# Kernel optimization log

Measured on AMD Instinct MI355X. Metric: run time of the kernel, lower is better.

## Reference

```python
import jax, jax.numpy as jnp
import numpy as np

B, N, T, F_IN, K, NUM_CLASSES = 32, 62, 1024, 5, 9, 3
CH = [F_IN, 32, 64, 128]
STRIDES = [1, 2, 1]
EPS = 1e-5  # torch InstanceNorm2d default eps


def setup_inputs() -> dict:
    key = jax.random.key(0)
    ks = jax.random.split(key, 32)
    ctr = [0]
    def nxt():
        k = ks[ctr[0]]; ctr[0] += 1; return k
    def nrm(shape, fan_in):
        return jax.random.normal(nxt(), shape, dtype=jnp.float32) / np.float32(np.sqrt(fan_in))
    inp = {}
    inp["x"] = jax.random.normal(nxt(), (B, N, T, F_IN), dtype=jnp.float32)
    # frozen learned graph: symmetric, non-negative, sparse-ish, zero diagonal
    a = jax.random.uniform(nxt(), (N, N), dtype=jnp.float32)
    a = jnp.maximum(jnp.tanh(a + a.T), 0.0)
    a = jnp.where(a > 0.8, a, 0.0)
    inp["adj"] = a * (1.0 - jnp.eye(N, dtype=jnp.float32))
    for i in range(3):
        cin, cout = CH[i], CH[i + 1]
        inp[f"gcn_w{i}"] = nrm((cin, cout), cin)
        inp[f"gcn_b{i}"] = jnp.zeros((cout,), jnp.float32)
        inp[f"conv_w{i}"] = nrm((cout, cout, 1, K), cout * K)
        inp[f"conv_b{i}"] = jnp.zeros((cout,), jnp.float32)
        inp[f"res_w{i}"] = nrm((cout, cin, 1, 1), cin)
        inp[f"res_b{i}"] = jnp.zeros((cout,), jnp.float32)
    inp["attn_w1"] = nrm((128, 64), 128)
    inp["attn_b1"] = jnp.zeros((64,), jnp.float32)
    inp["attn_w2"] = nrm((64, 1), 64)
    inp["attn_b2"] = jnp.zeros((1,), jnp.float32)
    inp["fc_w"] = nrm((128, NUM_CLASSES), 128)
    inp["fc_b"] = jnp.zeros((NUM_CLASSES,), jnp.float32)
    return inp


def _instance_norm(x):
    # InstanceNorm2d, affine=False: normalize per (sample, channel) over (node, time)
    m = jnp.mean(x, axis=(2, 3), keepdims=True)
    v = jnp.mean(jnp.square(x - m), axis=(2, 3), keepdims=True)
    return (x - m) * jax.lax.rsqrt(v + EPS)


def _conv(x, w, b, stride, pad):
    y = jax.lax.conv_general_dilated(
        x, w, window_strides=(1, stride), padding=[(0, 0), (pad, pad)],
        dimension_numbers=("NCHW", "OIHW", "NCHW"))
    return y + b[None, :, None, None]


def _block(x, a_norm, wg, bg, wc, bc, wr, br, stride):
    # residual 1x1 conv (always present: in!=out for every block here)
    res = _conv(x, wr, br, stride, 0)
    # GCNConv over all (batch, time) slices at once: A_norm @ (X W) + b
    y = jnp.einsum("bfnt,fo->bont", x, wg)
    y = jnp.einsum("mn,bont->bomt", a_norm, y) + bg[None, :, None, None]
    # TCN: IN -> ReLU -> Conv(1,K) -> IN -> ReLU (dropout = identity in eval)
    y = jax.nn.relu(_instance_norm(y))
    y = _conv(y, wc, bc, stride, (K - 1) // 2)
    y = jax.nn.relu(_instance_norm(y))
    return jax.nn.relu(y + res)


def _forward(x, adj, params, attn_w1, attn_b1, attn_w2, attn_b2, fc_w, fc_b):
    # symmetric GCN normalization with self loops (PyG gcn_norm on dense support)
    a_hat = adj + jnp.eye(N, dtype=adj.dtype)
    d = jnp.sum(a_hat, axis=1)
    dinv = jnp.where(d > 0, jax.lax.rsqrt(jnp.maximum(d, EPS)), 0.0)
    a_norm = dinv[:, None] * a_hat * dinv[None, :]
    h = jnp.transpose(x, (0, 3, 1, 2))  # (B, F, N, T)
    for i in range(3):
        h = _block(h, a_norm, *params[i], STRIDES[i])
    h = jnp.transpose(jnp.mean(h, axis=2), (0, 2, 1))  # (B, T', 128)
    hid = jnp.tanh(h @ attn_w1 + attn_b1)
    score = (hid @ attn_w2)[..., 0] + attn_b2[0]      # (B, T')
    w = jax.nn.softmax(score, axis=1)
    feat = jnp.einsum("btf,bt->bf", h, w)
    logits = feat @ fc_w + fc_b
    return logits, adj


def reference(x, adj,
              gcn_w0, gcn_b0, conv_w0, conv_b0, res_w0, res_b0,
              gcn_w1, gcn_b1, conv_w1, conv_b1, res_w1, res_b1,
              gcn_w2, gcn_b2, conv_w2, conv_b2, res_w2, res_b2,
              attn_w1, attn_b1, attn_w2, attn_b2, fc_w, fc_b):
    params = [
        (gcn_w0, gcn_b0, conv_w0, conv_b0, res_w0, res_b0),
        (gcn_w1, gcn_b1, conv_w1, conv_b1, res_w1, res_b1),
        (gcn_w2, gcn_b2, conv_w2, conv_b2, res_w2, res_b2),
    ]
    return _forward(x, adj, params, attn_w1, attn_b1, attn_w2, attn_b2, fc_w, fc_b)
```

## Files before the change

### kernel.cpp

```cpp
#include <hip/hip_runtime.h>


#define NN 62
#define KK 9

typedef short s16x8 __attribute__((ext_vector_type(8)));
typedef float f32x4 __attribute__((ext_vector_type(4)));

__device__ __forceinline__ unsigned short f2bf(float f) {
  unsigned u = __builtin_bit_cast(unsigned, f);
  u += 0x7FFF + ((u >> 16) & 1);
  return (unsigned short)(u >> 16);
}
__device__ __forceinline__ float bf2f(unsigned short u) {
  unsigned v = ((unsigned)u) << 16;
  return __builtin_bit_cast(float, v);
}
__device__ __forceinline__ ushort4 pack4(float4 a) {
  return (ushort4){f2bf(a.x), f2bf(a.y), f2bf(a.z), f2bf(a.w)};
}

__global__ __launch_bounds__(256) void k_prep(const float* __restrict__ adj,
                                              float* __restrict__ a_norm,
                                              float* __restrict__ out_adj) {
  __shared__ float dinv[NN];
  int tid = threadIdx.x;
  if (tid < NN) {
    float s = 1.0f;
    for (int n = 0; n < NN; n++) s += adj[tid * NN + n];
    dinv[tid] = (s > 0.f) ? rsqrtf(fmaxf(s, 1e-5f)) : 0.f;
  }
  __syncthreads();
  for (int idx = tid; idx < NN * NN; idx += 256) {
    int m = idx / NN, n = idx - m * NN;
    float ah = adj[idx] + ((m == n) ? 1.f : 0.f);
    a_norm[idx] = dinv[m] * ah * dinv[n];
    out_adj[idx] = adj[idx];
  }
}

__global__ __launch_bounds__(256) void k_an(const float* __restrict__ a_norm,
                                            unsigned short* __restrict__ anf) {
  int idx = blockIdx.x * 256 + threadIdx.x;
  if (idx >= 4096) return;
  int j = idx & 7;
  int l = (idx >> 3) & 63;
  int rest = idx >> 9;
  int cb = rest & 1;
  int ob = rest >> 1;
  int m = ob * 16 + (l & 15);
  int n = cb * 32 + (l >> 4) * 8 + j;
  anf[idx] = (m < NN && n < NN) ? f2bf(a_norm[m * NN + n]) : (unsigned short)0;
}

__global__ __launch_bounds__(256) void k_wt(const float* __restrict__ wc,
                                            unsigned short* __restrict__ wf, int C,
                                            const float* __restrict__ wr,
                                            float* __restrict__ wrt, int CIN) {
  int stride = gridDim.x * blockDim.x;
  int total = KK * C * C;
  int nCB = C / 32;
  for (int idx = blockIdx.x * blockDim.x + threadIdx.x; idx < total; idx += stride) {
    int j = idx & 7;
    int l = (idx >> 3) & 63;
    int rest = idx >> 9;
    int cb = rest % nCB;
    int rest2 = rest / nCB;
    int ob = rest2 % (C / 16);
    int k = rest2 / (C / 16);
    int o = ob * 16 + (l & 15);
    int ci = cb * 32 + (l >> 4) * 8 + j;
    wf[idx] = f2bf(wc[((size_t)o * C + ci) * KK + k]);
  }
  int t2 = C * CIN;
  for (int i = blockIdx.x * blockDim.x + threadIdx.x; i < t2; i += stride) {
    int o = i / CIN, ci = i - o * CIN;
    wrt[ci * C + o] = wr[i];
  }
}

__global__ __launch_bounds__(256) void k_wg(const float* __restrict__ gw,
                                            unsigned short* __restrict__ wgf,
                                            int CIN, int COUT, int KPAD) {
  int total = (COUT / 16) * (KPAD / 32) * 512;
  int stride = gridDim.x * blockDim.x;
  for (int idx = blockIdx.x * blockDim.x + threadIdx.x; idx < total; idx += stride) {
    int j = idx & 7;
    int l = (idx >> 3) & 63;
    int rest = idx >> 9;
    int cb = rest % (KPAD / 32);
    int ob = rest / (KPAD / 32);
    int o = ob * 16 + (l & 15);
    int f = cb * 32 + (l >> 4) * 8 + j;
    wgf[idx] = (f < CIN) ? f2bf(gw[(size_t)f * COUT + o]) : (unsigned short)0;
  }
}

__global__ __launch_bounds__(256) void k_xcast(const float* __restrict__ x,
                                               unsigned short* __restrict__ xb, int b0) {
  constexpr int TT2 = 256, TIN = 1024, CIN = 5;
  __shared__ float xt[TT2 * CIN];
  int t0 = blockIdx.x * TT2, n = blockIdx.y, bl = blockIdx.z;
  int tid = threadIdx.x;
  const float* xp = x + ((size_t)((b0 + bl) * NN + n) * TIN + t0) * CIN;
  for (int i = tid; i < TT2 * CIN; i += 256) xt[i] = xp[i];
  __syncthreads();
  for (int i = tid; i < CIN * TT2; i += 256) {
    int f = i / TT2, tl = i - f * TT2;
    xb[((size_t)bl * CIN + f) * NN * TIN + (size_t)n * TIN + t0 + tl] = f2bf(xt[tl * CIN + f]);
  }
}

template <int CIN, int TIN>
__global__ __launch_bounds__(256) void k_spatmma(const unsigned short* __restrict__ in,
                                                 const unsigned short* __restrict__ anf,
                                                 unsigned short* __restrict__ xs) {
  constexpr int BT = 256;
  constexpr int CP = 72;
  constexpr int BNP = BT + 8;
  constexpr int ZTSZ = BT * CP;
  constexpr int WLSZ = 4096;
  constexpr int OTSZ = 64 * BNP;
  constexpr int SH = (ZTSZ + WLSZ > OTSZ) ? ZTSZ + WLSZ : OTSZ;
  __shared__ unsigned short sh[SH];
  unsigned short* zt = sh;
  unsigned short* wl = sh + ZTSZ;

  int t0 = blockIdx.x * BT;
  int f = blockIdx.y;
  int bl = blockIdx.z;
  int tid = threadIdx.x;

  for (int i = tid * 4; i < WLSZ; i += 1024)
    *reinterpret_cast<ushort4*>(&wl[i]) = *reinterpret_cast<const ushort4*>(&anf[i]);

  const unsigned short* ib = in + ((size_t)bl * CIN + f) * (size_t)NN * TIN;
  for (int i = tid * 4; i < 64 * BT; i += 1024) {
    int n = i / BT, tl = i - n * BT;
    ushort4 u = {0, 0, 0, 0};
    if (n < NN) u = *reinterpret_cast<const ushort4*>(&ib[(size_t)n * TIN + t0 + tl]);
    unsigned short vv[4] = {u.x, u.y, u.z, u.w};
    int xo = ((tl >> 2) & 7) << 3;
#pragma unroll
    for (int j = 0; j < 4; j++) zt[(tl + j) * CP + (n ^ xo)] = vv[j];
  }
  __syncthreads();

  int w = tid >> 6;
  int lane = tid & 63;
  int lm = lane & 15, kh = lane >> 4;
  int col0 = w * 64;

  f32x4 acc[4][4];
#pragma unroll
  for (int mf = 0; mf < 4; mf++)
#pragma unroll
    for (int nf = 0; nf < 4; nf++) acc[mf][nf] = (f32x4){0.f, 0.f, 0.f, 0.f};

#pragma unroll
  for (int cb = 0; cb < 2; cb++) {
    s16x8 a[4], b[4];
#pragma unroll
    for (int mf = 0; mf < 4; mf++)
      a[mf] = *reinterpret_cast<const s16x8*>(&wl[(mf * 2 + cb) * 512 + lane * 8]);
#pragma unroll
    for (int nf = 0; nf < 4; nf++) {
      int col = col0 + nf * 16 + lm;
      int off = (cb * 32 + kh * 8) ^ (((col >> 2) & 7) << 3);
      b[nf] = *reinterpret_cast<const s16x8*>(&zt[col * CP + off]);
    }
#pragma unroll
    for (int mf = 0; mf < 4; mf++)
#pragma unroll
      for (int nf = 0; nf < 4; nf++)
        acc[mf][nf] = __builtin_amdgcn_mfma_f32_16x16x32_bf16(a[mf], b[nf], acc[mf][nf], 0, 0, 0);
  }

  __syncthreads();
  unsigned short* ot = sh;
#pragma unroll
  for (int mf = 0; mf < 4; mf++)
#pragma unroll
    for (int nf = 0; nf < 4; nf++) {
      int col = col0 + nf * 16 + lm;
#pragma unroll
      for (int rr = 0; rr < 4; rr++) {
        int m = mf * 16 + kh * 4 + rr;
        ot[m * BNP + col] = f2bf(acc[mf][nf][rr]);
      }
    }
  __syncthreads();
  for (int i = tid * 4; i < NN * BT; i += 1024) {
    int m = i / BT, col = i - m * BT;
    ushort4 v = *reinterpret_cast<const ushort4*>(&ot[m * BNP + col]);
    *reinterpret_cast<ushort4*>(&xs[(((size_t)bl * CIN + f) * NN + m) * TIN + t0 + col]) = v;
  }
}

template <int CIN, int COUT, int TIN>
__global__ __launch_bounds__(256) void k_wmixmma(const unsigned short* __restrict__ xs,
                                                 const unsigned short* __restrict__ wgf,
                                                 unsigned short* __restrict__ y,
                                                 float* __restrict__ part) {
  constexpr int S = NN * TIN;
  constexpr int KPAD = (CIN <= 32) ? 32 : 64;
  constexpr int CP = KPAD + 8;
  constexpr int BN = (COUT >= 128) ? 128 : 256;
  constexpr int BNP = BN + 8;
  constexpr int WM = (COUT >= 64) ? 2 : 1;
  constexpr int WN = 4 / WM;
  constexpr int MF = COUT / (16 * WM);
  constexpr int NF = BN / (16 * WN);
  constexpr int XM = (KPAD == 32) ? 3 : 7;
  constexpr int ZTSZ = BN * CP;
  constexpr int WLSZ = COUT * KPAD;
  constexpr int OTSZ = COUT * BNP;
  constexpr int SH = (ZTSZ + WLSZ > OTSZ) ? ZTSZ + WLSZ : OTSZ;
  __shared__ unsigned short sh[SH];
  unsigned short* zt = sh;
  unsigned short* wl = sh + ZTSZ;

  int s0 = blockIdx.x * BN;
  int bl = blockIdx.y;
  int tid = threadIdx.x;

  for (int i = tid * 4; i < WLSZ; i += 1024)
    *reinterpret_cast<ushort4*>(&wl[i]) = *reinterpret_cast<const ushort4*>(&wgf[i]);

  const unsigned short* xb = xs + (size_t)bl * CIN * S;
  for (int i = tid * 4; i < KPAD * BN; i += 1024) {
    int f = i / BN, sl = i - (i / BN) * BN;
    ushort4 u = {0, 0, 0, 0};
    if (f < CIN) u = *reinterpret_cast<const ushort4*>(&xb[(size_t)f * S + s0 + sl]);
    unsigned short vv[4] = {u.x, u.y, u.z, u.w};
#pragma unroll
    for (int j = 0; j < 4; j++) {
      int s_ = sl + j;
      zt[s_ * CP + (f ^ ((((s_) >> 2) & XM) << 3))] = vv[j];
    }
  }
  __syncthreads();

  int w = tid >> 6;
  int lane = tid & 63;
  int lm = lane & 15, kh = lane >> 4;
  int o0w = (w / WN) * (COUT / WM);
  int col0 = (w % WN) * (BN / WN);
  int obBase = o0w >> 4;

  f32x4 acc[MF][NF];
#pragma unroll
  for (int mf = 0; mf < MF; mf++)
#pragma unroll
    for (int nf = 0; nf < NF; nf++) acc[mf][nf] = (f32x4){0.f, 0.f, 0.f, 0.f};

#pragma unroll
  for (int cb = 0; cb < KPAD / 32; cb++) {
    s16x8 a[MF], b[NF];
#pragma unroll
    for (int mf = 0; mf < MF; mf++)
      a[mf] = *reinterpret_cast<const s16x8*>(&wl[((obBase + mf) * (KPAD / 32) + cb) * 512 + lane * 8]);
#pragma unroll
    for (int nf = 0; nf < NF; nf++) {
      int col = col0 + nf * 16 + lm;
      int off = (cb * 32 + kh * 8) ^ (((col >> 2) & XM) << 3);
      b[nf] = *reinterpret_cast<const s16x8*>(&zt[col * CP + off]);
    }
#pragma unroll
    for (int mf = 0; mf < MF; mf++)
#pragma unroll
      for (int nf = 0; nf < NF; nf++)
        acc[mf][nf] = __builtin_amdgcn_mfma_f32_16x16x32_bf16(a[mf], b[nf], acc[mf][nf], 0, 0, 0);
  }

  __syncthreads();
  unsigned short* ot = sh;
#pragma unroll
  for (int mf = 0; mf < MF; mf++)
#pragma unroll
    for (int nf = 0; nf < NF; nf++) {
      int col = col0 + nf * 16 + lm;
#pragma unroll
      for (int rr = 0; rr < 4; rr++) {
        int o = o0w + mf * 16 + kh * 4 + rr;
        ot[o * BNP + col] = f2bf(acc[mf][nf][rr]);
      }
    }
  __syncthreads();
  int NBLK = gridDim.x;
  constexpr int W = (BN / 4 < 64) ? BN / 4 : 64;
  for (int i = tid * 4; i < COUT * BN; i += 1024) {
    int o = i / BN, col = i - (i / BN) * BN;
    ushort4 v = *reinterpret_cast<const ushort4*>(&ot[o * BNP + col]);
    *reinterpret_cast<ushort4*>(&y[((size_t)bl * COUT + o) * S + s0 + col]) = v;
    float f0 = bf2f(v.x), f1 = bf2f(v.y), f2 = bf2f(v.z), f3 = bf2f(v.w);
    float s = f0 + f1 + f2 + f3;
    float s2 = f0 * f0 + f1 * f1 + f2 * f2 + f3 * f3;
    for (int off = W / 2; off; off >>= 1) {
      s += __shfl_down(s, off);
      s2 += __shfl_down(s2, off);
    }
    if ((tid & (W - 1)) == 0) {
      size_t po = (((size_t)bl * COUT + o) * NBLK + blockIdx.x) * 2;
      part[po] = s;
      part[po + 1] = s2;
    }
  }
}

__global__ __launch_bounds__(256) void k_statsR(const float* __restrict__ part,
                                                float* __restrict__ stats,
                                                int NBLK, float invS) {
  int c = blockIdx.x, C = gridDim.x, bl = blockIdx.y;
  const float* p = part + (((size_t)bl * C + c) * NBLK) * 2;
  float s = 0.f, s2 = 0.f;
  for (int i = threadIdx.x; i < NBLK; i += 256) {
    s += p[2 * i];
    s2 += p[2 * i + 1];
  }
  for (int off = 32; off; off >>= 1) {
    s += __shfl_down(s, off);
    s2 += __shfl_down(s2, off);
  }
  __shared__ float ls[4], ls2[4];
  int w = threadIdx.x >> 6;
  if ((threadIdx.x & 63) == 0) {
    ls[w] = s;
    ls2[w] = s2;
  }
  __syncthreads();
  if (threadIdx.x == 0) {
    float S1 = ls[0] + ls[1] + ls[2] + ls[3];
    float S2 = ls2[0] + ls2[1] + ls2[2] + ls2[3];
    float m = S1 * invS;
    float v = S2 * invS - m * m;
    stats[((size_t)bl * C + c) * 2 + 0] = m;
    stats[((size_t)bl * C + c) * 2 + 1] = rsqrtf(fmaxf(v, 0.f) + 1e-5f);
  }
}

template <int C, int TIN, int STRIDE, int BN>
__global__ __launch_bounds__(512) void k_convmma(const unsigned short* __restrict__ y,
                                                 const unsigned short* __restrict__ wf,
                                                 const float* __restrict__ statsY,
                                                 unsigned short* __restrict__ cbuf,
                                                 float* __restrict__ partC) {
  constexpr int TOUT = TIN / STRIDE;
  constexpr int SPAN = STRIDE * BN + 8;
  constexpr int CP = C + 8;
  constexpr int WM = (C >= 64) ? 2 : 1;
  constexpr int WN = 8 / WM;
  constexpr int MF = C / (16 * WM);
  constexpr int NF = BN / (16 * WN);
  constexpr int BNP = BN + 8;
  constexpr int XM = (C == 32) ? 3 : 7;
  constexpr bool ALLW = (C == 32);
  constexpr int WLSZ = ALLW ? C * C * KK : C * C;
  constexpr int WREGS = (C * C + 2047) / 2048;

  __shared__ unsigned short zt[SPAN * CP];
  __shared__ unsigned short wl[WLSZ];
  static_assert(C * BNP <= SPAN * CP, "epilogue stage must fit in zt");

  int t0 = blockIdx.x * BN;
  int n = blockIdx.y;
  int bl = blockIdx.z;
  int tid = threadIdx.x;
  int tin0 = STRIDE * t0 - 4;

  ushort4 wreg[WREGS];
  if (!ALLW) {
#pragma unroll
    for (int j = 0; j < WREGS; j++) {
      int idx = (tid + j * 512) * 4;
      if (idx < C * C) wreg[j] = *reinterpret_cast<const ushort4*>(&wf[idx]);
    }
  } else {
    for (int i = tid * 4; i < WLSZ; i += 2048)
      *reinterpret_cast<ushort4*>(&wl[i]) = *reinterpret_cast<const ushort4*>(&wf[i]);
  }

  const unsigned short* yb = y + ((size_t)bl * C) * NN * TIN + (size_t)n * TIN;
  const float* stY = statsY + (size_t)bl * 2 * C;
  for (int i = tid * 4; i < C * SPAN; i += 2048) {
    int ci = i / SPAN, r = i - ci * SPAN;
    int t = tin0 + r;
    const unsigned short* yrow = yb + (size_t)ci * NN * TIN;
    float m = stY[2 * ci], rs = stY[2 * ci + 1];
    float zv[4];
    if (t >= 0 && t + 4 <= TIN) {
      ushort4 u = *reinterpret_cast<const ushort4*>(&yrow[t]);
      zv[0] = fmaxf((bf2f(u.x) - m) * rs, 0.f);
      zv[1] = fmaxf((bf2f(u.y) - m) * rs, 0.f);
      zv[2] = fmaxf((bf2f(u.z) - m) * rs, 0.f);
      zv[3] = fmaxf((bf2f(u.w) - m) * rs, 0.f);
    } else {
#pragma unroll
      for (int j = 0; j < 4; j++) {
        int tj = t + j;
        zv[j] = (tj >= 0 && tj < TIN) ? fmaxf((bf2f(yrow[tj]) - m) * rs, 0.f) : 0.f;
      }
    }
    int xo = ((r >> 2) & XM) << 3;
#pragma unroll
    for (int j = 0; j < 4; j++) zt[(r + j) * CP + (ci ^ xo)] = f2bf(zv[j]);
  }
  if (!ALLW) {
#pragma unroll
    for (int j = 0; j < WREGS; j++) {
      int idx = (tid + j * 512) * 4;
      if (idx < C * C) *reinterpret_cast<ushort4*>(&wl[idx]) = wreg[j];
    }
  }

  int w = tid >> 6;
  int lane = tid & 63;
  int lm = lane & 15, kh = lane >> 4;
  int o0w = (w / WN) * (C / WM);
  int col0 = (w % WN) * (BN / WN);
  int obBase = o0w >> 4;

  f32x4 acc[MF][NF];
#pragma unroll
  for (int mf = 0; mf < MF; mf++)
#pragma unroll
    for (int nf = 0; nf < NF; nf++) acc[mf][nf] = (f32x4){0.f, 0.f, 0.f, 0.f};

  __syncthreads();

  for (int k = 0; k < KK; k++) {
    if (!ALLW && k + 1 < KK) {
      const unsigned short* wg = wf + (size_t)(k + 1) * C * C;
#pragma unroll
      for (int j = 0; j < WREGS; j++) {
        int idx = (tid + j * 512) * 4;
        if (idx < C * C) wreg[j] = *reinterpret_cast<const ushort4*>(&wg[idx]);
      }
    }
#pragma unroll
    for (int cb = 0; cb < C / 32; cb++) {
      s16x8 a[MF], b[NF];
#pragma unroll
      for (int mf = 0; mf < MF; mf++) {
        int base = ALLW ? ((k * (C / 16) + obBase + mf) * (C / 32) + cb) * 512
                        : ((obBase + mf) * (C / 32) + cb) * 512;
        a[mf] = *reinterpret_cast<const s16x8*>(&wl[base + lane * 8]);
      }
#pragma unroll
      for (int nf = 0; nf < NF; nf++) {
        int col = col0 + nf * 16 + lm;
        int r = STRIDE * col + k;
        int off = (cb * 32 + kh * 8) ^ (((r >> 2) & XM) << 3);
        b[nf] = *reinterpret_cast<const s16x8*>(&zt[r * CP + off]);
      }
#pragma unroll
      for (int mf = 0; mf < MF; mf++)
#pragma unroll
        for (int nf = 0; nf < NF; nf++)
          acc[mf][nf] = __builtin_amdgcn_mfma_f32_16x16x32_bf16(a[mf], b[nf], acc[mf][nf], 0, 0, 0);
    }
    if (!ALLW && k + 1 < KK) {
      __syncthreads();
#pragma unroll
      for (int j = 0; j < WREGS; j++) {
        int idx = (tid + j * 512) * 4;
        if (idx < C * C) *reinterpret_cast<ushort4*>(&wl[idx]) = wreg[j];
      }
      __syncthreads();
    }
  }

  __syncthreads();
  unsigned short* ot = zt;
#pragma unroll
  for (int mf = 0; mf < MF; mf++)
#pragma unroll
    for (int nf = 0; nf < NF; nf++) {
      int col = col0 + nf * 16 + lm;
#pragma unroll
      for (int rr = 0; rr < 4; rr++) {
        int o = o0w + mf * 16 + kh * 4 + rr;
        ot[o * BNP + col] = f2bf(acc[mf][nf][rr]);
      }
    }
  __syncthreads();
  int pb = blockIdx.y * gridDim.x + blockIdx.x;
  constexpr int W = (BN / 4 < 64) ? BN / 4 : 64;
  for (int i = tid * 4; i < C * BN; i += 2048) {
    int o = i / BN, col = i - (i / BN) * BN;
    ushort4 v = *reinterpret_cast<const ushort4*>(&ot[o * BNP + col]);
    *reinterpret_cast<ushort4*>(&cbuf[(((size_t)bl * C + o) * NN + n) * TOUT + t0 + col]) = v;
    float f0 = bf2f(v.x), f1 = bf2f(v.y), f2 = bf2f(v.z), f3 = bf2f(v.w);
    float s = f0 + f1 + f2 + f3;
    float s2 = f0 * f0 + f1 * f1 + f2 * f2 + f3 * f3;
    for (int off = W / 2; off; off >>= 1) {
      s += __shfl_down(s, off);
      s2 += __shfl_down(s2, off);
    }
    if ((tid & (W - 1)) == 0) {
      size_t po = (((size_t)bl * C + o) * 248 + pb) * 2;
      partC[po] = s;
      partC[po + 1] = s2;
    }
  }
}

template <int CIN, int COUT, int TOUT, int STRIDE, bool LAYX>
__global__ __launch_bounds__(256) void k_post(const unsigned short* __restrict__ cbuf,
                                              const float* __restrict__ statsC,
                                              const void* __restrict__ in,
                                              const float* __restrict__ wrt,
                                              const float* __restrict__ br,
                                              unsigned short* __restrict__ out, int b0) {
  constexpr int TT = 64;
  constexpr int TIN_ = TOUT * STRIDE;
  __shared__ float inT[CIN * TT];
  __shared__ float wL[CIN * COUT];
  __shared__ float brL[COUT];
  __shared__ float stL[2 * COUT];
  int t0 = blockIdx.x * TT, n = blockIdx.y, bl = blockIdx.z;
  int tid = threadIdx.x;
  for (int i = tid; i < CIN * COUT; i += 256) wL[i] = wrt[i];
  if (tid < COUT) brL[tid] = br[tid];
  for (int i = tid; i < 2 * COUT; i += 256) stL[i] = statsC[(size_t)bl * 2 * COUT + i];
  for (int i = tid; i < CIN * TT; i += 256) {
    int ci = i / TT, tl = i - ci * TT;
    int t = STRIDE * (t0 + tl);
    float v;
    if (LAYX)
      v = ((const float*)in)[(((size_t)(b0 + bl) * NN + n) * TIN_ + t) * CIN + ci];
    else
      v = bf2f(((const unsigned short*)in)[(((size_t)bl * CIN + ci) * NN + n) * TIN_ + t]);
    inT[i] = v;
  }
  __syncthreads();
  int tl = tid & 63;
  int o4 = tid >> 6;
  int t = t0 + tl;
  for (int op = 0; op < COUT / 16; op++) {
    int o0 = op * 16 + o4 * 4;
    float accA[4] = {0.f, 0.f, 0.f, 0.f};
    for (int ci = 0; ci < CIN; ci++) {
      float xv = inT[ci * TT + tl];
      float4 wv = *reinterpret_cast<const float4*>(&wL[ci * COUT + o0]);
      accA[0] += wv.x * xv;
      accA[1] += wv.y * xv;
      accA[2] += wv.z * xv;
      accA[3] += wv.w * xv;
    }
#pragma unroll
    for (int q = 0; q < 4; q++) {
      int o = o0 + q;
      float m = stL[2 * o], rs = stL[2 * o + 1];
      float cv = bf2f(cbuf[(((size_t)bl * COUT + o) * NN + n) * TOUT + t]);
      float v = fmaxf((cv - m) * rs, 0.f) + accA[q] + brL[o];
      out[(((size_t)bl * COUT + o) * NN + n) * TOUT + t] = f2bf(fmaxf(v, 0.f));
    }
  }
}

__global__ __launch_bounds__(256) void k_pool(const unsigned short* __restrict__ src,
                                              float* __restrict__ pooled, int b0) {
  constexpr int CP2 = 128, TPZ = 512;
  int t = blockIdx.x * 64 + (threadIdx.x & 63);
  int c = blockIdx.y * 4 + (threadIdx.x >> 6);
  int bl = blockIdx.z;
  const unsigned short* p = src + ((size_t)bl * CP2 + c) * NN * TPZ + t;
  float s = 0.f;
  for (int n = 0; n < NN; n++) s += bf2f(p[(size_t)n * TPZ]);
  pooled[((size_t)(b0 + bl) * TPZ + t) * CP2 + c] = s * (1.f / NN);
}

__global__ __launch_bounds__(128) void k_attn1(const float* __restrict__ pooled,
                                               const float* __restrict__ w1,
                                               const float* __restrict__ b1,
                                               const float* __restrict__ w2,
                                               const float* __restrict__ b2v,
                                               float* __restrict__ score) {
  __shared__ float w1L[128 * 64];
  __shared__ float w2L[64];
  __shared__ float b1L[64];
  int b = blockIdx.y;
  int t = blockIdx.x * 128 + threadIdx.x;
  int tid = threadIdx.x;
  for (int i = tid; i < 128 * 64; i += 128) w1L[i] = w1[i];
  if (tid < 64) {
    w2L[tid] = w2[tid];
    b1L[tid] = b1[tid];
  }
  __syncthreads();
  float hid[64];
#pragma unroll
  for (int j = 0; j < 64; j++) hid[j] = b1L[j];
  const float* pv = &pooled[((size_t)b * 512 + t) * 128];
  for (int c = 0; c < 128; c++) {
    float xv = pv[c];
#pragma unroll
    for (int j = 0; j < 64; j++) hid[j] += xv * w1L[c * 64 + j];
  }
  float s = b2v[0];
#pragma unroll
  for (int j = 0; j < 64; j++) s += tanhf(hid[j]) * w2L[j];
  score[(size_t)b * 512 + t] = s;
}

__global__ __launch_bounds__(256) void k_attn2(const float* __restrict__ score,
                                               float* __restrict__ wgt) {
  __shared__ float sc[512];
  __shared__ float red[4];
  int b = blockIdx.x;
  int tid = threadIdx.x;
  for (int t = tid; t < 512; t += 256) sc[t] = score[(size_t)b * 512 + t];
  __syncthreads();
  float mx = -1e30f;
  for (int t = tid; t < 512; t += 256) mx = fmaxf(mx, sc[t]);
  for (int off = 32; off; off >>= 1) mx = fmaxf(mx, __shfl_down(mx, off));
  if ((tid & 63) == 0) red[tid >> 6] = mx;
  __syncthreads();
  mx = fmaxf(fmaxf(red[0], red[1]), fmaxf(red[2], red[3]));
  __syncthreads();
  float sum = 0.f;
  for (int t = tid; t < 512; t += 256) {
    float e = expf(sc[t] - mx);
    sc[t] = e;
    sum += e;
  }
  for (int off = 32; off; off >>= 1) sum += __shfl_down(sum, off);
  if ((tid & 63) == 0) red[tid >> 6] = sum;
  __syncthreads();
  float inv = 1.f / (red[0] + red[1] + red[2] + red[3]);
  for (int t = tid; t < 512; t += 256) wgt[(size_t)b * 512 + t] = sc[t] * inv;
}

__global__ __launch_bounds__(256) void k_feat2(const float* __restrict__ pooled,
                                               const float* __restrict__ wgt,
                                               float* __restrict__ featb) {
  __shared__ float sh[16][17];
  int b = blockIdx.y;
  int c0 = blockIdx.x * 16;
  int cl = threadIdx.x & 15, tlane = threadIdx.x >> 4;
  float s = 0.f;
  for (int t = tlane; t < 512; t += 16)
    s += pooled[((size_t)b * 512 + t) * 128 + c0 + cl] * wgt[(size_t)b * 512 + t];
  sh[tlane][cl] = s;
  __syncthreads();
  if (threadIdx.x < 16) {
    float a = 0.f;
    for (int q = 0; q < 16; q++) a += sh[q][threadIdx.x];
    featb[(size_t)b * 128 + c0 + threadIdx.x] = a;
  }
}

__global__ __launch_bounds__(128) void k_logits(const float* __restrict__ featb,
                                                const float* __restrict__ fcw,
                                                const float* __restrict__ fcb,
                                                float* __restrict__ out) {
  __shared__ float fL[128];
  int b = blockIdx.x;
  fL[threadIdx.x] = featb[(size_t)b * 128 + threadIdx.x];
  __syncthreads();
  if (threadIdx.x < 3) {
    float l = fcb[threadIdx.x];
    for (int cc = 0; cc < 128; cc++) l += fL[cc] * fcw[cc * 3 + threadIdx.x];
    out[(size_t)b * 3 + threadIdx.x] = l;
  }
}

extern "C" void kernel_launch(void* const* d_in, const int* in_sizes, int n_in,
                              void* d_out, int out_size, void* d_ws, size_t ws_size,
                              hipStream_t stream) {
  (void)in_sizes; (void)n_in; (void)out_size;
  const float* x = (const float*)d_in[0];
  const float* adj = (const float*)d_in[1];
  const float* gw0 = (const float*)d_in[2];
  const float* cw0 = (const float*)d_in[4];
  const float* rw0 = (const float*)d_in[6];
  const float* rb0 = (const float*)d_in[7];
  const float* gw1 = (const float*)d_in[8];
  const float* cw1 = (const float*)d_in[10];
  const float* rw1 = (const float*)d_in[12];
  const float* rb1 = (const float*)d_in[13];
  const float* gw2 = (const float*)d_in[14];
  const float* cw2 = (const float*)d_in[16];
  const float* rw2 = (const float*)d_in[18];
  const float* rb2 = (const float*)d_in[19];
  const float* aw1 = (const float*)d_in[20];
  const float* ab1 = (const float*)d_in[21];
  const float* aw2 = (const float*)d_in[22];
  const float* ab2 = (const float*)d_in[23];
  const float* fcw = (const float*)d_in[24];
  const float* fcb = (const float*)d_in[25];
  float* out = (float*)d_out;
  float* ws = (float*)d_ws;

  float* a_norm = ws;
  unsigned short* wk0 = (unsigned short*)(a_norm + 3844);
  unsigned short* wk1 = (unsigned short*)(a_norm + 8452);
  unsigned short* wk2 = (unsigned short*)(a_norm + 26884);
  float* wrt0 = a_norm + 100612;
  float* wrt1 = a_norm + 100772;
  float* wrt2 = a_norm + 102820;
  unsigned short* wg0f = (unsigned short*)(a_norm + 111012);
  unsigned short* wg1f = (unsigned short*)(a_norm + 111524);
  unsigned short* wg2f = (unsigned short*)(a_norm + 112548);
  unsigned short* anf = (unsigned short*)(a_norm + 116644);
  float* pooled = a_norm + 118692;
  float* scoreb = pooled + 2097152;
  float* wgtA = scoreb + 16384;
  float* featb = wgtA + 16384;
  float* chunk_base = featb + 4096;
  size_t shared_floats = (size_t)(chunk_base - ws);

  const size_t PS_BUF = 2031616;
  const size_t PS_P1 = 131072;
  const size_t PS_P2 = 65536;
  const size_t per_sample = 3 * PS_BUF + PS_P1 + PS_P2 + 512;

  size_t avail = ws_size / sizeof(float);
  long cap = 1;
  if (avail > shared_floats) cap = (long)((avail - shared_floats) / per_sample);
  int Bc = (int)cap;
  if (Bc < 1) Bc = 1;
  if (Bc > 32) Bc = 32;

  k_prep<<<dim3(1), dim3(256), 0, stream>>>(adj, a_norm, out + 96);
  k_an<<<dim3(16), dim3(256), 0, stream>>>(a_norm, anf);
  k_wt<<<dim3(64), dim3(256), 0, stream>>>(cw0, wk0, 32, rw0, wrt0, 5);
  k_wt<<<dim3(160), dim3(256), 0, stream>>>(cw1, wk1, 64, rw1, wrt1, 32);
  k_wt<<<dim3(576), dim3(256), 0, stream>>>(cw2, wk2, 128, rw2, wrt2, 64);
  k_wg<<<dim3(4), dim3(256), 0, stream>>>(gw0, wg0f, 5, 32, 32);
  k_wg<<<dim3(8), dim3(256), 0, stream>>>(gw1, wg1f, 32, 64, 32);
  k_wg<<<dim3(32), dim3(256), 0, stream>>>(gw2, wg2f, 64, 128, 64);

  float* sp1 = chunk_base;
  float* sp2 = sp1 + (size_t)Bc * PS_P1;
  float* stY = sp2 + (size_t)Bc * PS_P2;
  float* stC = stY + (size_t)Bc * 256;
  float* B1 = stC + (size_t)Bc * 256;
  float* B2 = B1 + (size_t)Bc * PS_BUF;
  float* B3 = B2 + (size_t)Bc * PS_BUF;

  for (int b0 = 0; b0 < 32; b0 += Bc) {
    int bc = (32 - b0 < Bc) ? (32 - b0) : Bc;
    unsigned short* B1u = (unsigned short*)B1;
    unsigned short* B2u = (unsigned short*)B2;
    unsigned short* B3u = (unsigned short*)B3;

    k_xcast<<<dim3(4, NN, bc), dim3(256), 0, stream>>>(x, B1u, b0);
    k_spatmma<5, 1024><<<dim3(4, 5, bc), dim3(256), 0, stream>>>(B1u, anf, B2u);
    k_wmixmma<5, 32, 1024><<<dim3(248, bc), dim3(256), 0, stream>>>(B2u, wg0f, B3u, sp1);
    k_statsR<<<dim3(32, bc), dim3(256), 0, stream>>>(sp1, stY, 248, 1.f / 63488.f);
    k_convmma<32, 1024, 1, 256><<<dim3(4, NN, bc), dim3(512), 0, stream>>>(B3u, wk0, stY, B2u, sp2);
    k_statsR<<<dim3(32, bc), dim3(256), 0, stream>>>(sp2, stC, 248, 1.f / 63488.f);
    k_post<5, 32, 1024, 1, true><<<dim3(16, NN, bc), dim3(256), 0, stream>>>(
        B2u, stC, x, wrt0, rb0, B1u, b0);

    k_spatmma<32, 1024><<<dim3(4, 32, bc), dim3(256), 0, stream>>>(B1u, anf, B3u);
    k_wmixmma<32, 64, 1024><<<dim3(248, bc), dim3(256), 0, stream>>>(B3u, wg1f, B2u, sp1);
    k_statsR<<<dim3(64, bc), dim3(256), 0, stream>>>(sp1, stY, 248, 1.f / 63488.f);
    k_convmma<64, 1024, 2, 128><<<dim3(4, NN, bc), dim3(512), 0, stream>>>(B2u, wk1, stY, B3u, sp2);
    k_statsR<<<dim3(64, bc), dim3(256), 0, stream>>>(sp2, stC, 248, 1.f / 31744.f);
    k_post<32, 64, 512, 2, false><<<dim3(8, NN, bc), dim3(256), 0, stream>>>(
        B3u, stC, B1u, wrt1, rb1, B2u, b0);

    k_spatmma<64, 512><<<dim3(2, 64, bc), dim3(256), 0, stream>>>(B2u, anf, B1u);
    k_wmixmma<64, 128, 512><<<dim3(248, bc), dim3(256), 0, stream>>>(B1u, wg2f, B3u, sp1);
    k_statsR<<<dim3(128, bc), dim3(256), 0, stream>>>(sp1, stY, 248, 1.f / 31744.f);
    k_convmma<128, 512, 1, 128><<<dim3(4, NN, bc), dim3(512), 0, stream>>>(B3u, wk2, stY, B1u, sp2);
    k_statsR<<<dim3(128, bc), dim3(256), 0, stream>>>(sp2, stC, 248, 1.f / 31744.f);
    k_post<64, 128, 512, 1, false><<<dim3(8, NN, bc), dim3(256), 0, stream>>>(
        B1u, stC, B2u, wrt2, rb2, B3u, b0);

    k_pool<<<dim3(8, 32, bc), dim3(256), 0, stream>>>(B3u, pooled, b0);
  }

  k_attn1<<<dim3(4, 32), dim3(128), 0, stream>>>(pooled, aw1, ab1, aw2, ab2, scoreb);
  k_attn2<<<dim3(32), dim3(256), 0, stream>>>(scoreb, wgtA);
  k_feat2<<<dim3(8, 32), dim3(256), 0, stream>>>(pooled, wgtA, featb);
  k_logits<<<dim3(32), dim3(128), 0, stream>>>(featb, fcw, fcb, out);
}
```

Measured before the change: 2.391 ms.

## Use MFMA for residual post kernels and stream conv weights from global

Adds a k_postmma kernel that computes the 1x1 residual convolution with bf16 MFMA on LDS-staged inputs, fused with the instance-norm, ReLU, bias and residual-add epilogue. It replaces the scalar k_post for blocks 1 and 2, using residual weights pre-packed into MFMA fragment layout by a new k_wr kernel. Separately, k_convmma no longer stages weights in LDS with barriers per tap. Each wave now loads its A fragments straight from global memory with one-step register prefetch. This removes LDS weight traffic and the per-tap syncs, at the cost of more global/L2 loads per wave.

```diff
diff --git a/kernel.cpp b/kernel.cpp
--- a/kernel.cpp
+++ b/kernel.cpp
@@ -93,6 +93,23 @@
     int o = ob * 16 + (l & 15);
     int f = cb * 32 + (l >> 4) * 8 + j;
     wgf[idx] = (f < CIN) ? f2bf(gw[(size_t)f * COUT + o]) : (unsigned short)0;
+  }
+}
+
+__global__ __launch_bounds__(256) void k_wr(const float* __restrict__ wr,
+                                            unsigned short* __restrict__ wrf,
+                                            int CIN, int COUT, int KPAD) {
+  int total = (COUT / 16) * (KPAD / 32) * 512;
+  int stride = gridDim.x * blockDim.x;
+  for (int idx = blockIdx.x * blockDim.x + threadIdx.x; idx < total; idx += stride) {
+    int j = idx & 7;
+    int l = (idx >> 3) & 63;
+    int rest = idx >> 9;
+    int cb = rest % (KPAD / 32);
+    int ob = rest / (KPAD / 32);
+    int o = ob * 16 + (l & 15);
+    int f = cb * 32 + (l >> 4) * 8 + j;
+    wrf[idx] = (f < CIN) ? f2bf(wr[(size_t)o * CIN + f]) : (unsigned short)0;
   }
 }
 
@@ -354,12 +371,10 @@
   constexpr int NF = BN / (16 * WN);
   constexpr int BNP = BN + 8;
   constexpr int XM = (C == 32) ? 3 : 7;
-  constexpr bool ALLW = (C == 32);
-  constexpr int WLSZ = ALLW ? C * C * KK : C * C;
-  constexpr int WREGS = (C * C + 2047) / 2048;
+  constexpr int NCB = C / 32;
+  constexpr int IT = KK * NCB;
 
   __shared__ unsigned short zt[SPAN * CP];
-  __shared__ unsigned short wl[WLSZ];
   static_assert(C * BNP <= SPAN * CP, "epilogue stage must fit in zt");
 
   int t0 = blockIdx.x * BN;
@@ -368,17 +383,18 @@
   int tid = threadIdx.x;
   int tin0 = STRIDE * t0 - 4;
 
-  ushort4 wreg[WREGS];
-  if (!ALLW) {
-#pragma unroll
-    for (int j = 0; j < WREGS; j++) {
-      int idx = (tid + j * 512) * 4;
-      if (idx < C * C) wreg[j] = *reinterpret_cast<const ushort4*>(&wf[idx]);
-    }
-  } else {
-    for (int i = tid * 4; i < WLSZ; i += 2048)
-      *reinterpret_cast<ushort4*>(&wl[i]) = *reinterpret_cast<const ushort4*>(&wf[i]);
-  }
+  int w = tid >> 6;
+  int lane = tid & 63;
+  int lm = lane & 15, kh = lane >> 4;
+  int o0w = (w / WN) * (C / WM);
+  int col0 = (w % WN) * (BN / WN);
+  int obBase = o0w >> 4;
+
+  s16x8 acur[MF], anxt[MF];
+#pragma unroll
+  for (int mf = 0; mf < MF; mf++)
+    acur[mf] = *reinterpret_cast<const s16x8*>(
+        &wf[(((size_t)(obBase + mf)) * NCB) * 512 + lane * 8]);
 
   const unsigned short* yb = y + ((size_t)bl * C) * NN * TIN + (size_t)n * TIN;
   const float* stY = statsY + (size_t)bl * 2 * C;
@@ -405,20 +421,6 @@
 #pragma unroll
     for (int j = 0; j < 4; j++) zt[(r + j) * CP + (ci ^ xo)] = f2bf(zv[j]);
   }
-  if (!ALLW) {
-#pragma unroll
-    for (int j = 0; j < WREGS; j++) {
-      int idx = (tid + j * 512) * 4;
-      if (idx < C * C) *reinterpret_cast<ushort4*>(&wl[idx]) = wreg[j];
-    }
-  }
-
-  int w = tid >> 6;
-  int lane = tid & 63;
-  int lm = lane & 15, kh = lane >> 4;
-  int o0w = (w / WN) * (C / WM);
-  int col0 = (w % WN) * (BN / WN);
-  int obBase = o0w >> 4;
 
   f32x4 acc[MF][NF];
 #pragma unroll
@@ -428,45 +430,32 @@
 
   __syncthreads();
 
-  for (int k = 0; k < KK; k++) {
-    if (!ALLW && k + 1 < KK) {
-      const unsigned short* wg = wf + (size_t)(k + 1) * C * C;
-#pragma unroll
-      for (int j = 0; j < WREGS; j++) {
-        int idx = (tid + j * 512) * 4;
-        if (idx < C * C) wreg[j] = *reinterpret_cast<const ushort4*>(&wg[idx]);
-      }
-    }
-#pragma unroll
-    for (int cb = 0; cb < C / 32; cb++) {
-      s16x8 a[MF], b[NF];
-#pragma unroll
-      for (int mf = 0; mf < MF; mf++) {
-        int base = ALLW ? ((k * (C / 16) + obBase + mf) * (C / 32) + cb) * 512
-                        : ((obBase + mf) * (C / 32) + cb) * 512;
-        a[mf] = *reinterpret_cast<const s16x8*>(&wl[base + lane * 8]);
-      }
-#pragma unroll
-      for (int nf = 0; nf < NF; nf++) {
-        int col = col0 + nf * 16 + lm;
-        int r = STRIDE * col + k;
-        int off = (cb * 32 + kh * 8) ^ (((r >> 2) & XM) << 3);
-        b[nf] = *reinterpret_cast<const s16x8*>(&zt[r * CP + off]);
-      }
+  for (int it = 0; it < IT; ++it) {
+    int k = it / NCB, cb = it - (it / NCB) * NCB;
+    if (it + 1 < IT) {
+      int it2 = it + 1;
+      int k2 = it2 / NCB, cb2 = it2 - (it2 / NCB) * NCB;
 #pragma unroll
       for (int mf = 0; mf < MF; mf++)
-#pragma unroll
-        for (int nf = 0; nf < NF; nf++)
-          acc[mf][nf] = __builtin_amdgcn_mfma_f32_16x16x32_bf16(a[mf], b[nf], acc[mf][nf], 0, 0, 0);
-    }
-    if (!ALLW && k + 1 < KK) {
-      __syncthreads();
-#pragma unroll
-      for (int j = 0; j < WREGS; j++) {
-        int idx = (tid + j * 512) * 4;
-        if (idx < C * C) *reinterpret_cast<ushort4*>(&wl[idx]) = wreg[j];
-      }
-      __syncthreads();
+        anxt[mf] = *reinterpret_cast<const s16x8*>(
+            &wf[((((size_t)k2 * (C / 16) + obBase + mf) * NCB + cb2) << 9) + lane * 8]);
+    }
+    s16x8 b[NF];
+#pragma unroll
+    for (int nf = 0; nf < NF; nf++) {
+      int col = col0 + nf * 16 + lm;
+      int r = STRIDE * col + k;
+      int off = (cb * 32 + kh * 8) ^ (((r >> 2) & XM) << 3);
+      b[nf] = *reinterpret_cast<const s16x8*>(&zt[r * CP + off]);
+    }
+#pragma unroll
+    for (int mf = 0; mf < MF; mf++)
+#pragma unroll
+      for (int nf = 0; nf < NF; nf++)
+        acc[mf][nf] = __builtin_amdgcn_mfma_f32_16x16x32_bf16(acur[mf], b[nf], acc[mf][nf], 0, 0, 0);
+    if (it + 1 < IT) {
+#pragma unroll
+      for (int mf = 0; mf < MF; mf++) acur[mf] = anxt[mf];
     }
   }
 
@@ -502,6 +491,129 @@
       partC[po] = s;
       partC[po + 1] = s2;
     }
+  }
+}
+
+template <int CIN, int COUT, int TOUT, int STRIDE>
+__global__ __launch_bounds__(256) void k_postmma(const unsigned short* __restrict__ cbuf,
+                                                 const float* __restrict__ statsC,
+                                                 const unsigned short* __restrict__ in,
+                                                 const unsigned short* __restrict__ wrf,
+                                                 const float* __restrict__ br,
+                                                 unsigned short* __restrict__ out) {
+  constexpr int BN = 128;
+  constexpr int TIN_ = TOUT * STRIDE;
+  constexpr int KPAD = (CIN <= 32) ? 32 : 64;
+  constexpr int CP = KPAD + 8;
+  constexpr int BNP = BN + 8;
+  constexpr int MF = COUT / 32;
+  constexpr int NF = 4;
+  constexpr int XM = (KPAD == 32) ? 3 : 7;
+  constexpr int ZTSZ = BN * CP;
+  constexpr int WLSZ = COUT * KPAD;
+  constexpr int OTSZ = COUT * BNP;
+  constexpr int SH = (ZTSZ + WLSZ > OTSZ) ? ZTSZ + WLSZ : OTSZ;
+  __shared__ unsigned short sh[SH];
+  __shared__ float stL[2 * COUT];
+  __shared__ float brL[COUT];
+  unsigned short* zt = sh;
+  unsigned short* wl = sh + ZTSZ;
+
+  int t0 = blockIdx.x * BN;
+  int n = blockIdx.y;
+  int bl = blockIdx.z;
+  int tid = threadIdx.x;
+
+  for (int i = tid; i < 2 * COUT; i += 256) stL[i] = statsC[(size_t)bl * 2 * COUT + i];
+  if (tid < COUT) brL[tid] = br[tid];
+
+  for (int i = tid * 4; i < WLSZ; i += 1024)
+    *reinterpret_cast<ushort4*>(&wl[i]) = *reinterpret_cast<const ushort4*>(&wrf[i]);
+
+  const unsigned short* ib = in + ((size_t)bl * CIN) * NN * TIN_ + (size_t)n * TIN_;
+  for (int i = tid * 4; i < KPAD * BN; i += 1024) {
+    int f = i / BN, sl = i - (i / BN) * BN;
+    unsigned short vv[4] = {0, 0, 0, 0};
+    if (f < CIN) {
+      const unsigned short* row = ib + (size_t)f * NN * TIN_;
+      if (STRIDE == 1) {
+        ushort4 u = *reinterpret_cast<const ushort4*>(&row[t0 + sl]);
+        vv[0] = u.x; vv[1] = u.y; vv[2] = u.z; vv[3] = u.w;
+      } else {
+        ushort4 u0 = *reinterpret_cast<const ushort4*>(&row[2 * (t0 + sl)]);
+        ushort4 u1 = *reinterpret_cast<const ushort4*>(&row[2 * (t0 + sl) + 4]);
+        vv[0] = u0.x; vv[1] = u0.z; vv[2] = u1.x; vv[3] = u1.z;
+      }
+    }
+#pragma unroll
+    for (int j = 0; j < 4; j++) {
+      int s_ = sl + j;
+      zt[s_ * CP + (f ^ ((((s_) >> 2) & XM) << 3))] = vv[j];
+    }
+  }
+  __syncthreads();
+
+  int w = tid >> 6;
+  int lane = tid & 63;
+  int lm = lane & 15, kh = lane >> 4;
+  int o0w = (w / 2) * (COUT / 2);
+  int col0 = (w % 2) * 64;
+  int obBase = o0w >> 4;
+
+  f32x4 acc[MF][NF];
+#pragma unroll
+  for (int mf = 0; mf < MF; mf++)
+#pragma unroll
+    for (int nf = 0; nf < NF; nf++) acc[mf][nf] = (f32x4){0.f, 0.f, 0.f, 0.f};
+
+#pragma unroll
+  for (int cb = 0; cb < KPAD / 32; cb++) {
+    s16x8 a[MF], b[NF];
+#pragma unroll
+    for (int mf = 0; mf < MF; mf++)
+      a[mf] = *reinterpret_cast<const s16x8*>(&wl[((obBase + mf) * (KPAD / 32) + cb) * 512 + lane * 8]);
+#pragma unroll
+    for (int nf = 0; nf < NF; nf++) {
+      int col = col0 + nf * 16 + lm;
+      int off = (cb * 32 + kh * 8) ^ (((col >> 2) & XM) << 3);
+      b[nf] = *reinterpret_cast<const s16x8*>(&zt[col * CP + off]);
+    }
+#pragma unroll
+    for (int mf = 0; mf < MF; mf++)
+#pragma unroll
+      for (int nf = 0; nf < NF; nf++)
+        acc[mf][nf] = __builtin_amdgcn_mfma_f32_16x16x32_bf16(a[mf], b[nf], acc[mf][nf], 0, 0, 0);
+  }
+
+  __syncthreads();
+  unsigned short* ot = sh;
+#pragma unroll
+  for (int mf = 0; mf < MF; mf++)
+#pragma unroll
+    for (int nf = 0; nf < NF; nf++) {
+      int col = col0 + nf * 16 + lm;
+#pragma unroll
+      for (int rr = 0; rr < 4; rr++) {
+        int o = o0w + mf * 16 + kh * 4 + rr;
+        ot[o * BNP + col] = f2bf(acc[mf][nf][rr]);
+      }
+    }
+  __syncthreads();
+  for (int i = tid * 4; i < COUT * BN; i += 1024) {
+    int o = i / BN, col = i - (i / BN) * BN;
+    ushort4 rv = *reinterpret_cast<const ushort4*>(&ot[o * BNP + col]);
+    ushort4 cv = *reinterpret_cast<const ushort4*>(&cbuf[(((size_t)bl * COUT + o) * NN + n) * TOUT + t0 + col]);
+    float m = stL[2 * o], rs = stL[2 * o + 1], bb = brL[o];
+    ushort4 ov;
+    float v0 = fmaxf((bf2f(cv.x) - m) * rs, 0.f) + bf2f(rv.x) + bb;
+    float v1 = fmaxf((bf2f(cv.y) - m) * rs, 0.f) + bf2f(rv.y) + bb;
+    float v2 = fmaxf((bf2f(cv.z) - m) * rs, 0.f) + bf2f(rv.z) + bb;
+    float v3 = fmaxf((bf2f(cv.w) - m) * rs, 0.f) + bf2f(rv.w) + bb;
+    ov.x = f2bf(fmaxf(v0, 0.f));
+    ov.y = f2bf(fmaxf(v1, 0.f));
+    ov.z = f2bf(fmaxf(v2, 0.f));
+    ov.w = f2bf(fmaxf(v3, 0.f));
+    *reinterpret_cast<ushort4*>(&out[(((size_t)bl * COUT + o) * NN + n) * TOUT + t0 + col]) = ov;
   }
 }
 
@@ -704,7 +816,9 @@
   unsigned short* wg1f = (unsigned short*)(a_norm + 111524);
   unsigned short* wg2f = (unsigned short*)(a_norm + 112548);
   unsigned short* anf = (unsigned short*)(a_norm + 116644);
-  float* pooled = a_norm + 118692;
+  unsigned short* wr1f = (unsigned short*)(a_norm + 118692);
+  unsigned short* wr2f = (unsigned short*)(a_norm + 119716);
+  float* pooled = a_norm + 123812;
   float* scoreb = pooled + 2097152;
   float* wgtA = scoreb + 16384;
   float* featb = wgtA + 16384;
@@ -731,6 +845,8 @@
   k_wg<<<dim3(4), dim3(256), 0, stream>>>(gw0, wg0f, 5, 32, 32);
   k_wg<<<dim3(8), dim3(256), 0, stream>>>(gw1, wg1f, 32, 64, 32);
   k_wg<<<dim3(32), dim3(256), 0, stream>>>(gw2, wg2f, 64, 128, 64);
+  k_wr<<<dim3(8), dim3(256), 0, stream>>>(rw1, wr1f, 32, 64, 32);
+  k_wr<<<dim3(32), dim3(256), 0, stream>>>(rw2, wr2f, 64, 128, 64);
 
   float* sp1 = chunk_base;
   float* sp2 = sp1 + (size_t)Bc * PS_P1;
@@ -760,16 +876,16 @@
     k_statsR<<<dim3(64, bc), dim3(256), 0, stream>>>(sp1, stY, 248, 1.f / 63488.f);
     k_convmma<64, 1024, 2, 128><<<dim3(4, NN, bc), dim3(512), 0, stream>>>(B2u, wk1, stY, B3u, sp2);
     k_statsR<<<dim3(64, bc), dim3(256), 0, stream>>>(sp2, stC, 248, 1.f / 31744.f);
-    k_post<32, 64, 512, 2, false><<<dim3(8, NN, bc), dim3(256), 0, stream>>>(
-        B3u, stC, B1u, wrt1, rb1, B2u, b0);
+    k_postmma<32, 64, 512, 2><<<dim3(4, NN, bc), dim3(256), 0, stream>>>(
+        B3u, stC, B1u, wr1f, rb1, B2u);
 
     k_spatmma<64, 512><<<dim3(2, 64, bc), dim3(256), 0, stream>>>(B2u, anf, B1u);
     k_wmixmma<64, 128, 512><<<dim3(248, bc), dim3(256), 0, stream>>>(B1u, wg2f, B3u, sp1);
     k_statsR<<<dim3(128, bc), dim3(256), 0, stream>>>(sp1, stY, 248, 1.f / 31744.f);
     k_convmma<128, 512, 1, 128><<<dim3(4, NN, bc), dim3(512), 0, stream>>>(B3u, wk2, stY, B1u, sp2);
     k_statsR<<<dim3(128, bc), dim3(256), 0, stream>>>(sp2, stC, 248, 1.f / 31744.f);
-    k_post<64, 128, 512, 1, false><<<dim3(8, NN, bc), dim3(256), 0, stream>>>(
-        B1u, stC, B2u, wrt2, rb2, B3u, b0);
+    k_postmma<64, 128, 512, 1><<<dim3(4, NN, bc), dim3(256), 0, stream>>>(
+        B1u, stC, B2u, wr2f, rb2, B3u);
 
     k_pool<<<dim3(8, 32, bc), dim3(256), 0, stream>>>(B3u, pooled, b0);
   }
```

After: 2.039 ms. -14.7%, faster.
